# Optimization experiments

Hardware: AMD Instinct MI355X
Metric: run time of the kernel (lower is better)

The kernel has to match this reference:

```python
import jax, jax.numpy as jnp
import numpy as np

B, L, IN_DIM, D, H = 4, 1024, 256, 512, 8
DH = D // H
LARGE_NEG = -10000.0
LN_EPS = 1e-5


def _layernorm(x, g, b):
    mu = jnp.mean(x, axis=-1, keepdims=True)
    var = jnp.mean((x - mu) ** 2, axis=-1, keepdims=True)
    return (x - mu) * jax.lax.rsqrt(var + LN_EPS) * g + b


def setup_inputs() -> dict:
    key = jax.random.key(0)
    ks = jax.random.split(key, 16)
    s = 0.02
    return {
        "x": jax.random.normal(ks[0], (B, L, IN_DIM), jnp.float32),
        "attention_mask": jax.random.bernoulli(ks[1], 0.5, (B, L, L)),
        "adjacency_matrix": jax.random.uniform(ks[2], (B, L, L), jnp.float32),
        "W_fuse": jax.random.normal(ks[3], (D, IN_DIM), jnp.float32) * s,
        "b_fuse": jnp.zeros((D,), jnp.float32),
        "in_proj_w": jax.random.normal(ks[4], (3 * D, D), jnp.float32) * s,
        "in_proj_b": jnp.zeros((3 * D,), jnp.float32),
        "out_w": jax.random.normal(ks[5], (D, D), jnp.float32) * s,
        "out_b": jnp.zeros((D,), jnp.float32),
        "ln1_g": jnp.ones((D,), jnp.float32),
        "ln1_b": jnp.zeros((D,), jnp.float32),
        "ln2_g": jnp.ones((D,), jnp.float32),
        "ln2_b": jnp.zeros((D,), jnp.float32),
        "W1": jax.random.normal(ks[6], (4 * D, D), jnp.float32) * s,
        "b1": jnp.zeros((4 * D,), jnp.float32),
        "W2": jax.random.normal(ks[7], (D, 4 * D), jnp.float32) * s,
        "b2": jnp.zeros((D,), jnp.float32),
        "log_scale": jnp.array(0.0, jnp.float32),  # log(adj_bias_strength=1.0)
    }


def reference(x, attention_mask, adjacency_matrix, W_fuse, b_fuse, in_proj_w,
              in_proj_b, out_w, out_b, ln1_g, ln1_b, ln2_g, ln2_b,
              W1, b1, W2, b2, log_scale):
    # fuse projection (in_dim != d_model)
    x = jnp.einsum("bli,di->bld", x, W_fuse) + b_fuse

    # ensure_self_loops_in_mask: unmask diagonal of fully-masked rows
    eye = jnp.eye(L, dtype=bool)
    row_all = jnp.all(attention_mask, axis=-1)  # [B, L]
    mask = attention_mask & ~(eye[None, :, :] & row_all[:, :, None])

    # additive attention bias: large_neg where masked + scaled clipped adjacency
    bias = jnp.where(mask, LARGE_NEG, 0.0) + \
        jnp.exp(log_scale) * jnp.clip(adjacency_matrix, 0.0, 1.0)  # [B, L, L]

    # --- attention block (pre-norm) ---
    x_norm = _layernorm(x, ln1_g, ln1_b)
    qkv = jnp.einsum("bld,ed->ble", x_norm, in_proj_w) + in_proj_b
    q, k, v = jnp.split(qkv, 3, axis=-1)
    q = q.reshape(B, L, H, DH).transpose(0, 2, 1, 3)  # [B,H,L,DH]
    k = k.reshape(B, L, H, DH).transpose(0, 2, 1, 3)
    v = v.reshape(B, L, H, DH).transpose(0, 2, 1, 3)
    scores = jnp.einsum("bhqd,bhkd->bhqk", q, k) / np.sqrt(DH) + bias[:, None]
    probs = jax.nn.softmax(scores, axis=-1)
    ctx = jnp.einsum("bhqk,bhkd->bhqd", probs, v)
    ctx = ctx.transpose(0, 2, 1, 3).reshape(B, L, D)
    attn_out = jnp.einsum("bld,ed->ble", ctx, out_w) + out_b
    x = x + attn_out

    # --- FFN block (pre-norm) ---
    x_norm = _layernorm(x, ln2_g, ln2_b)
    h = jax.nn.gelu(jnp.einsum("bld,fd->blf", x_norm, W1) + b1, approximate=False)
    ff = jnp.einsum("blf,df->bld", h, W2) + b2
    return x + ff
```

## Files before the change

### kernel.cpp

```cpp
#include <hip/hip_runtime.h>
#include <math.h>

typedef unsigned short UST;
typedef __attribute__((ext_vector_type(8))) short bf16x8;
typedef __attribute__((ext_vector_type(4))) float f32x4;

#define BB 4
#define LL 1024
#define IND 256
#define DD 512
#define HH 8
#define FFD 2048
#define NT (BB*LL)

__device__ __forceinline__ float bf2f(UST u){ return __uint_as_float(((unsigned)u)<<16); }
__device__ __forceinline__ UST f2bf(float f){
  unsigned u = __float_as_uint(f);
  u += 0x7FFFu + ((u>>16)&1u);
  return (UST)(u>>16);
}
__device__ __forceinline__ float ldF(const void* p, long i, int isf32){
  return isf32 ? ((const float*)p)[i] : bf2f(((const UST*)p)[i]);
}
__device__ __forceinline__ bool ldMask(const void* p, long i, int fm){
  if (fm==0) return ((const int*)p)[i] != 0;
  if (fm==1) return ((const unsigned char*)p)[i] != 0;
  if (fm==2) return ((const UST*)p)[i] != 0;
  return ((const float*)p)[i] != 0.f;
}
__device__ __forceinline__ f32x4 mfma16(bf16x8 a, bf16x8 b, f32x4 c){
  return __builtin_amdgcn_mfma_f32_16x16x32_bf16(a, b, c, 0, 0, 0);
}
__device__ __forceinline__ void gld16(const void* g, void* l){
  __builtin_amdgcn_global_load_lds((const __attribute__((address_space(1))) unsigned int*)g,
                                   (__attribute__((address_space(3))) unsigned int*)l, 16, 0, 0);
}

struct CvtArgs { const void* src[11]; UST* dst[11]; int n[11]; };
__global__ __launch_bounds__(256) void prep_k(int* flags, CvtArgs a,
    const UST* xh, const void* mask, const void* adj, const void* lsp, UST* biasOut){
  int bid = blockIdx.x;
  int t = threadIdx.x;
  __shared__ UST sTile[1024];
  __shared__ int sAll[4];
  __shared__ int sFlags[2];
  if (t < 64){
    int lane = t;
    int e0 = (xh[lane] >> 7) & 0xFF;
    int e1 = (xh[64+lane] >> 7) & 0xFF;
    int f32 = __any((e0 >= 140) || (e1 >= 140)) ? 1 : 0;
    unsigned v = ((const unsigned int*)mask)[lane];
    int w01   = __all(v <= 1u) ? 1 : 0;
    unsigned lo = v & 0xFFFFu, hi = v >> 16;
    int half  = __all((lo==0u||lo==0x3F80u) && (hi==0u||hi==0x3F80u)) ? 1 : 0;
    int wordF = __all(v==0u || v==0x3F800000u) ? 1 : 0;
    int byteB = __all((v & 0xFEFEFEFEu) == 0u) ? 1 : 0;
    if (lane == 0){
      int fm = w01 ? 0 : (half ? (wordF ? 3 : 2) : (byteB ? 1 : 0));
      sFlags[0] = f32; sFlags[1] = fm;
      if (bid == 0){ flags[0] = f32; flags[1] = fm; }
    }
  }
  __syncthreads();
  int fF = sFlags[0], fM = sFlags[1];
  if (bid < BB*LL){
    int row = bid;
    int i = row & (LL-1);
    long base = (long)row * LL;
    int j0 = t*4;
    bool mv[4];
    if (fM == 0){
      int4 m4 = *(const int4*)((const int*)mask + base + j0);
      mv[0]=m4.x!=0; mv[1]=m4.y!=0; mv[2]=m4.z!=0; mv[3]=m4.w!=0;
    } else {
      #pragma unroll
      for (int k=0;k<4;++k) mv[k] = ldMask(mask, base + j0 + k, fM);
    }
    float a4[4];
    if (fF){
      float4 av = *(const float4*)((const float*)adj + base + j0);
      a4[0]=av.x; a4[1]=av.y; a4[2]=av.z; a4[3]=av.w;
    } else {
      const UST* ap = (const UST*)adj + base + j0;
      #pragma unroll
      for (int k=0;k<4;++k) a4[k] = bf2f(ap[k]);
    }
    int my = (mv[0]&&mv[1]&&mv[2]&&mv[3]) ? 1 : 0;
    int wa = __all(my);
    int w = t >> 6;
    if ((t & 63) == 0) sAll[w] = wa;
    __syncthreads();
    int rowAll = sAll[0] & sAll[1] & sAll[2] & sAll[3];
    float es = expf(ldF(lsp, 0, fF));
    UST o4[4];
    #pragma unroll
    for (int k = 0; k < 4; ++k){
      int j = j0 + k;
      float av = fminf(fmaxf(a4[k], 0.f), 1.f);
      bool eff = mv[k] && !((rowAll != 0) && (j == i));
      o4[k] = f2bf(((eff ? -10000.f : 0.f) + es * av) * 1.44269504f);
    }
    *(int2*)&sTile[j0] = *(const int2*)o4;
    __syncthreads();
    int kt = t >> 4, l15 = t & 15;
    UST g4[4];
    #pragma unroll
    for (int ni=0; ni<4; ++ni) g4[ni] = sTile[kt*64 + ni*16 + l15];
    int b = row >> 10, rr = row & 1023;
    int qt = rr >> 6, q = rr & 63;
    int w2 = q >> 4, qd = (q >> 2) & 3, r = q & 3;
    long dst = ((long)((b*16 + qt)*16 + kt))*4096 + w2*1024 + (qd*16 + l15)*16 + r*4;
    *(int2*)(biasOut + dst) = *(const int2*)g4;
  } else {
    int cb = bid - BB*LL;
    int ti = cb >> 9, xi = cb & 511;
    int n = a.n[ti];
    long i8 = ((long)xi*256 + t)*8;
    if (i8 >= n) return;
    const void* s = a.src[ti]; UST* d = a.dst[ti];
    if (fF){
      const float4* sf = (const float4*)s;
      float4 a0 = sf[i8>>2], a1 = sf[(i8>>2)+1];
      UST o[8] = { f2bf(a0.x),f2bf(a0.y),f2bf(a0.z),f2bf(a0.w),
                   f2bf(a1.x),f2bf(a1.y),f2bf(a1.z),f2bf(a1.w) };
      *(int4*)(d+i8) = *(const int4*)o;
    } else {
      ((int4*)d)[i8>>3] = ((const int4*)s)[i8>>3];
    }
  }
}

template<int TM, int TN, int ACT, int RES, int OUTMODE>
__global__ __launch_bounds__(256) void gemm3_k(const int* flags,
    const UST* __restrict__ A, const UST* __restrict__ Bw, const UST* __restrict__ bias,
    const float* __restrict__ resid, void* Cout, int M, int N, int K, int Ks){
  constexpr int MI = TM/32, NI = TN/32;
  __shared__ UST sA[2][TM*64];
  __shared__ UST sB[2][TN*64];
  int t = threadIdx.x, w = t>>6, lane = t&63, l15 = lane&15, qd = lane>>4;
  int m0 = blockIdx.x*TM, n0 = blockIdx.y*TN;
  int zoff = blockIdx.z * Ks;
  int wm = (w&1)*(TM/2), wn = (w>>1)*(TN/2);
  f32x4 acc[MI][NI];
  #pragma unroll
  for (int mi=0; mi<MI; ++mi)
    #pragma unroll
    for (int ni=0; ni<NI; ++ni){ acc[mi][ni][0]=0;acc[mi][ni][1]=0;acc[mi][ni][2]=0;acc[mi][ni][3]=0; }
  int sRow = lane&7, sCol = (lane>>3)*8;
  const UST* aS = A + (long)(m0 + w*(TM/4) + sRow)*K + sCol + zoff;
  const UST* bS = Bw + (long)(n0 + w*(TN/4) + sRow)*K + sCol + zoff;
  auto stage = [&](int buf, int k0){
    #pragma unroll
    for (int c=0;c<MI;++c) gld16(aS + (long)c*8*K + k0, (char*)&sA[buf][(w*(TM/4)+c*8)*64]);
    #pragma unroll
    for (int c=0;c<NI;++c) gld16(bS + (long)c*8*K + k0, (char*)&sB[buf][(w*(TN/4)+c*8)*64]);
  };
  stage(0, 0);
  for (int k0 = 0; k0 < Ks; k0 += 64){
    int cur = (k0>>6)&1, nxt = cur^1;
    __syncthreads();
    if (k0 + 64 < Ks) stage(nxt, k0+64);
    #pragma unroll
    for (int ks=0; ks<2; ++ks){
      bf16x8 afr[MI], bfr[NI];
      #pragma unroll
      for (int mi=0; mi<MI; ++mi){
        int R = wm + mi*16 + l15;
        afr[mi] = *(const bf16x8*)&sA[cur][(R>>3)*512 + (ks*4+qd)*64 + (R&7)*8];
      }
      #pragma unroll
      for (int ni=0; ni<NI; ++ni){
        int R = wn + ni*16 + l15;
        bfr[ni] = *(const bf16x8*)&sB[cur][(R>>3)*512 + (ks*4+qd)*64 + (R&7)*8];
      }
      #pragma unroll
      for (int mi=0; mi<MI; ++mi)
        #pragma unroll
        for (int ni=0; ni<NI; ++ni)
          acc[mi][ni] = mfma16(afr[mi], bfr[ni], acc[mi][ni]);
    }
  }
  if (OUTMODE == 3){
    float* P = (float*)Cout + (size_t)blockIdx.z * M * N;
    #pragma unroll
    for (int mi=0; mi<MI; ++mi)
      #pragma unroll
      for (int ni=0; ni<NI; ++ni){
        int gc = n0 + wn + ni*16 + l15;
        #pragma unroll
        for (int r=0; r<4; ++r){
          int grow = m0 + wm + mi*16 + qd*4 + r;
          P[(long)grow*N + gc] = acc[mi][ni][r];
        }
      }
    return;
  }
  int outF32 = (OUTMODE==1) || (OUTMODE==2 && flags[0]);
  #pragma unroll
  for (int mi=0; mi<MI; ++mi){
    #pragma unroll
    for (int ni=0; ni<NI; ++ni){
      int gc = n0 + wn + ni*16 + l15;
      float bv = bf2f(bias[gc]);
      #pragma unroll
      for (int r=0; r<4; ++r){
        int grow = m0 + wm + mi*16 + qd*4 + r;
        float c = acc[mi][ni][r] + bv;
        if (ACT) c = 0.5f*c*(1.f+erff(c*0.70710678118654752f));
        long oi = (long)grow*N + gc;
        if (RES) c += resid[oi];
        if (outF32) ((float*)Cout)[oi] = c;
        else ((UST*)Cout)[oi] = f2bf(c);
      }
    }
  }
}

__global__ __launch_bounds__(256) void reduce4_k(const int* flags,
    const float* __restrict__ parts, const UST* __restrict__ bias,
    const float* __restrict__ resid, void* __restrict__ dout){
  const long S = (long)NT*DD;
  long e = ((long)blockIdx.x*256 + threadIdx.x)*4;
  float4 a = *(const float4*)(parts + e);
  float4 b = *(const float4*)(parts + S + e);
  float4 c = *(const float4*)(parts + 2*S + e);
  float4 d = *(const float4*)(parts + 3*S + e);
  float4 r = *(const float4*)(resid + e);
  int gc = (int)(e & (DD-1));
  float v[4] = { a.x+b.x+c.x+d.x + bf2f(bias[gc+0]) + r.x,
                 a.y+b.y+c.y+d.y + bf2f(bias[gc+1]) + r.y,
                 a.z+b.z+c.z+d.z + bf2f(bias[gc+2]) + r.z,
                 a.w+b.w+c.w+d.w + bf2f(bias[gc+3]) + r.w };
  if (flags[0]){
    *(float4*)((float*)dout + e) = *(const float4*)v;
  } else {
    UST o4[4] = { f2bf(v[0]), f2bf(v[1]), f2bf(v[2]), f2bf(v[3]) };
    *(int2*)((UST*)dout + e) = *(const int2*)o4;
  }
}

__global__ __launch_bounds__(256) void ln_k(const int* flags, const float* xin,
    const void* gp, const void* bp, UST* xout){
  int fF = flags[0];
  int row = blockIdx.x, t = threadIdx.x;
  const float* xr = xin + (long)row * DD;
  float v0 = xr[t], v1 = xr[t+256];
  float s = v0+v1, q = v0*v0 + v1*v1;
  #pragma unroll
  for (int off=1; off<64; off<<=1){ s += __shfl_xor(s,off,64); q += __shfl_xor(q,off,64); }
  __shared__ float rs[4], rq[4];
  int w = t>>6;
  if ((t&63)==0){ rs[w]=s; rq[w]=q; }
  __syncthreads();
  float S = rs[0]+rs[1]+rs[2]+rs[3];
  float Q = rq[0]+rq[1]+rq[2]+rq[3];
  float mean = S * (1.f/DD);
  float var  = fmaxf(Q * (1.f/DD) - mean*mean, 0.f);
  float ri = rsqrtf(var + 1e-5f);
  float g0 = ldF(gp, t, fF), b0 = ldF(bp, t, fF);
  float g1 = ldF(gp, t+256, fF), b1 = ldF(bp, t+256, fF);
  xout[(long)row*DD + t]     = f2bf((v0-mean)*ri*g0 + b0);
  xout[(long)row*DD + t+256] = f2bf((v1-mean)*ri*g1 + b1);
}

__global__ __launch_bounds__(256) void repack_v(const UST* __restrict__ qkv, UST* __restrict__ vT){
  int id = blockIdx.x;
  int bh = id & 31, qt = id >> 5;
  int b = bh >> 3, h = bh & 7;
  int t = threadIdx.x, w = t >> 6, lane = t & 63;
  int token = qt*64 + lane;
  const UST* src = qkv + ((long)(b*LL + token))*1536 + 1024 + h*64;
  #pragma unroll
  for (int c = 0; c < 2; ++c){
    int ch = w*2 + c;
    union { int4 v; UST u[8]; } uu;
    uu.v = *(const int4*)(src + ch*8);
    #pragma unroll
    for (int i = 0; i < 8; ++i)
      vT[((long)(bh*64 + ch*8 + i))*LL + token] = uu.u[i];
  }
}

__global__ __launch_bounds__(256) void attn_k(const UST* __restrict__ qkv,
    const UST* __restrict__ vT, const UST* __restrict__ bias2, UST* __restrict__ ctx){
  int id = blockIdx.x;
  int b = id & 3, h = (id>>2) & 7, qt = id >> 5;
  int bh = b*HH + h;
  int q0 = qt*64;
  int t = threadIdx.x, w = t>>6, lane = t&63, l15 = lane&15, qd = lane>>4;
  __shared__ UST sK[2][2][64*32];
  __shared__ UST sV[2][2][64*32];
  __shared__ UST sP[4][16*72];
  UST* myP = &sP[w][0];

  const UST* qrow = qkv + ((long)(b*LL + q0 + w*16 + l15))*1536 + h*64;
  bf16x8 qf0 = *(const bf16x8*)(qrow + qd*8);
  bf16x8 qf1 = *(const bf16x8*)(qrow + 32 + qd*8);

  const UST* kS = qkv + (long)(b*LL + w*16 + (lane&15))*1536 + 512 + h*64 + (lane>>4)*8;
  const UST* vS = vT + (long)(bh*64 + w*16 + (lane&15))*LL + (lane>>4)*8;
  const UST* bP = bias2 + ((long)((b*16 + qt)*16))*4096 + w*1024 + lane*16;

  f32x4 o[4]; float lsum[4];
  #pragma unroll
  for (int i=0;i<4;i++){ o[i][0]=0;o[i][1]=0;o[i][2]=0;o[i][3]=0; lsum[i]=0.f; }
  const float C1 = 0.18033688f;

  auto stage = [&](int buf, int k0){
    gld16(kS + (long)k0*1536,      (char*)sK[buf][0] + w*1024);
    gld16(kS + (long)k0*1536 + 32, (char*)sK[buf][1] + w*1024);
    gld16(vS + k0,                 (char*)sV[buf][0] + w*1024);
    gld16(vS + k0 + 32,            (char*)sV[buf][1] + w*1024);
  };
  stage(0, 0);
  int4 bc0 = *(const int4*)(bP);
  int4 bc1 = *(const int4*)(bP + 8);

  for (int kt = 0; kt < 16; ++kt){
    int cur = kt&1, nxt = cur^1;
    int k0 = kt*64;
    __syncthreads();
    if (kt < 15) stage(nxt, k0+64);
    int kn = (kt < 15 ? kt+1 : 15);
    int4 bn0 = *(const int4*)(bP + (long)kn*4096);
    int4 bn1 = *(const int4*)(bP + (long)kn*4096 + 8);
    f32x4 s4[4];
    #pragma unroll
    for (int i=0;i<4;i++){ s4[i][0]=0;s4[i][1]=0;s4[i][2]=0;s4[i][3]=0; }
    #pragma unroll
    for (int ni=0; ni<4; ++ni){
      bf16x8 kf0 = *(const bf16x8*)&sK[cur][0][ni*512 + qd*128 + l15*8];
      bf16x8 kf1 = *(const bf16x8*)&sK[cur][1][ni*512 + qd*128 + l15*8];
      s4[ni] = mfma16(qf0, kf0, s4[ni]);
      s4[ni] = mfma16(qf1, kf1, s4[ni]);
    }
    union { int4 v; UST u[8]; } B0, B1;
    B0.v = bc0; B1.v = bc1;
    float p[4][4];
    #pragma unroll
    for (int ni=0; ni<4; ++ni){
      #pragma unroll
      for (int r=0; r<4; ++r){
        UST bu = (r < 2) ? B0.u[r*4 + ni] : B1.u[(r&1)*4 + ni];
        p[ni][r] = exp2f(fmaf(s4[ni][r], C1, bf2f(bu)));
      }
    }
    bc0 = bn0; bc1 = bn1;
    #pragma unroll
    for (int r=0; r<4; ++r)
      lsum[r] += (p[0][r]+p[1][r]) + (p[2][r]+p[3][r]);
    #pragma unroll
    for (int ni=0; ni<4; ++ni)
      #pragma unroll
      for (int r=0; r<4; ++r) myP[(qd*4+r)*72 + ni*16 + l15] = f2bf(p[ni][r]);
    bf16x8 pf0 = *(const bf16x8*)&myP[l15*72 + qd*8];
    bf16x8 pf1 = *(const bf16x8*)&myP[l15*72 + 32 + qd*8];
    #pragma unroll
    for (int dn=0; dn<4; ++dn){
      bf16x8 vf0 = *(const bf16x8*)&sV[cur][0][dn*512 + qd*128 + l15*8];
      bf16x8 vf1 = *(const bf16x8*)&sV[cur][1][dn*512 + qd*128 + l15*8];
      o[dn] = mfma16(pf0, vf0, o[dn]);
      o[dn] = mfma16(pf1, vf1, o[dn]);
    }
  }
  float linv[4];
  #pragma unroll
  for (int r=0; r<4; ++r){
    float s = lsum[r];
    #pragma unroll
    for (int off=1; off<16; off<<=1) s += __shfl_xor(s, off, 64);
    linv[r] = 1.f / s;
  }
  #pragma unroll
  for (int dn=0; dn<4; ++dn){
    #pragma unroll
    for (int r=0; r<4; ++r){
      long oi = ((long)(b*LL + q0 + w*16 + qd*4 + r))*DD + h*64 + dn*16 + l15;
      ctx[oi] = f2bf(o[dn][r] * linv[r]);
    }
  }
}

extern "C" void kernel_launch(void* const* d_in, const int* in_sizes, int n_in,
                              void* d_out, int out_size, void* d_ws, size_t ws_size,
                              hipStream_t stream){
  char* ws = (char*)d_ws;
  size_t o = 0;
  auto alloc = [&](size_t b){ size_t r = o; o += (b + 255) & ~(size_t)255; return r; };
  int*   flags = (int*)(ws + alloc(256));
  size_t biasOff = alloc(8UL<<20);
  size_t qkvOff  = alloc(12UL<<20);
  UST* biasC = (UST*)(ws + biasOff);
  UST* qkv   = (UST*)(ws + qkvOff);
  UST* hb    = (UST*)(ws + biasOff);
  UST* vT    = (UST*)(ws + alloc(4UL<<20));
  UST* xbf   = (UST*)(ws + alloc(2UL<<20));
  UST* wfuse = (UST*)(ws + alloc(131072*2));
  UST* bfuse = (UST*)(ws + alloc(1024));
  UST* ipw   = (UST*)(ws + alloc(786432*2));
  UST* ipb   = (UST*)(ws + alloc(3072*2));
  UST* outw  = (UST*)(ws + alloc(262144*2));
  UST* outb  = (UST*)(ws + alloc(1024));
  UST* w1    = (UST*)(ws + alloc(1048576*2));
  UST* b1    = (UST*)(ws + alloc(4096*2));
  UST* w2    = (UST*)(ws + alloc(1048576*2));
  UST* b2    = (UST*)(ws + alloc(1024));
  float* xf  = (float*)(ws + alloc((size_t)NT*DD*4));
  UST* xn    = (UST*)(ws + alloc((size_t)NT*DD*2));
  UST* ctx   = (UST*)(ws + alloc((size_t)NT*DD*2));
  float* x2  = (float*)(ws + alloc((size_t)NT*DD*4));
  size_t partsOff = alloc(4UL*NT*DD*4);
  float* parts = (float*)(ws + partsOff);
  bool doSplit = (o <= ws_size);

  CvtArgs ca;
  const int srcIdx[11] = {0,3,4,5,6,7,8,13,14,15,16};
  UST* dsts[11] = {xbf,wfuse,bfuse,ipw,ipb,outw,outb,w1,b1,w2,b2};
  const int ns[11] = {NT*IND, DD*IND, DD, 3*DD*DD, 3*DD, DD*DD, DD, FFD*DD, FFD, DD*FFD, DD};
  for (int i=0;i<11;i++){ ca.src[i]=d_in[srcIdx[i]]; ca.dst[i]=dsts[i]; ca.n[i]=ns[i]; }
  prep_k<<<BB*LL + 11*512, 256, 0, stream>>>(flags, ca, (const UST*)d_in[0],
                                             d_in[1], d_in[2], d_in[17], biasC);

  gemm3_k<64,64,0,0,1><<<dim3(64,8), 256, 0, stream>>>(flags, xbf, wfuse, bfuse, nullptr, xf, NT, DD, IND, IND);
  ln_k<<<NT, 256, 0, stream>>>(flags, xf, d_in[9], d_in[10], xn);
  gemm3_k<64,128,0,0,0><<<dim3(64,12), 256, 0, stream>>>(flags, xn, ipw, ipb, nullptr, qkv, NT, 3*DD, DD, DD);
  repack_v<<<512, 256, 0, stream>>>(qkv, vT);
  attn_k<<<512, 256, 0, stream>>>(qkv, vT, biasC, ctx);
  gemm3_k<64,64,0,1,1><<<dim3(64,8), 256, 0, stream>>>(flags, ctx, outw, outb, xf, x2, NT, DD, DD, DD);
  ln_k<<<NT, 256, 0, stream>>>(flags, x2, d_in[11], d_in[12], xn);
  gemm3_k<128,128,1,0,0><<<dim3(32,16), 256, 0, stream>>>(flags, xn, w1, b1, nullptr, hb, NT, FFD, DD, DD);
  if (doSplit){
    gemm3_k<128,128,0,0,3><<<dim3(32,4,4), 256, 0, stream>>>(flags, hb, w2, b2, nullptr, parts, NT, DD, FFD, FFD/4);
    reduce4_k<<<(NT*DD)/1024, 256, 0, stream>>>(flags, parts, b2, x2, d_out);
  } else {
    gemm3_k<64,64,0,1,2><<<dim3(64,8), 256, 0, stream>>>(flags, hb, w2, b2, x2, d_out, NT, DD, FFD, FFD);
  }
}
```

Baseline: 262.3 us.

## Fuse all stages into one cooperative persistent kernel with grid syncs

Replaces the chain of separate kernel launches (prep, GEMMs, layernorms, V repack, attention, split-K reduce) with a single cooperative kernel of 512 blocks. The stages are separated by grid-wide barriers, and each block works through its share of tiles using a shared 64KB LDS buffer. The aim is to remove per-launch overhead and the inter-kernel gaps. In exchange, a fixed 512-block grid with launch_bounds(256,2) caps occupancy, every grid.sync costs a barrier, and stages with more natural tiles (e.g. prep with ~9.7k rows) become strided loops. The old multi-kernel path stays as a fallback if the cooperative launch fails.

```diff
diff --git a/kernel.cpp b/kernel.cpp
--- a/kernel.cpp
+++ b/kernel.cpp
@@ -1,5 +1,8 @@
 #include <hip/hip_runtime.h>
+#include <hip/hip_cooperative_groups.h>
 #include <math.h>
+
+namespace cg = cooperative_groups;
 
 typedef unsigned short UST;
 typedef __attribute__((ext_vector_type(8))) short bf16x8;
@@ -36,52 +39,61 @@
                                    (__attribute__((address_space(3))) unsigned int*)l, 16, 0, 0);
 }
 
-struct CvtArgs { const void* src[11]; UST* dst[11]; int n[11]; };
-__global__ __launch_bounds__(256) void prep_k(int* flags, CvtArgs a,
-    const UST* xh, const void* mask, const void* adj, const void* lsp, UST* biasOut){
-  int bid = blockIdx.x;
+struct MegaArgs {
+  const void* src[11]; UST* dst[11]; int n[11];
+  const UST* xh; const void* mask; const void* adj; const void* lsp;
+  const void* ln1g; const void* ln1b; const void* ln2g; const void* ln2b;
+  UST *bias2, *qkv, *vT, *xn, *ctx, *hb;
+  UST *xbf, *wfuse, *bfuse, *ipw, *ipb, *outw, *outb, *w1, *b1, *w2, *b2;
+  float *xf, *x2, *parts;
+  void* dout;
+  int* flags;
+};
+
+__device__ __forceinline__ void detect_dev(const UST* xh, const unsigned int* mw, int* sF){
   int t = threadIdx.x;
-  __shared__ UST sTile[1024];
-  __shared__ int sAll[4];
-  __shared__ int sFlags[2];
   if (t < 64){
-    int lane = t;
-    int e0 = (xh[lane] >> 7) & 0xFF;
-    int e1 = (xh[64+lane] >> 7) & 0xFF;
+    int e0 = (xh[t] >> 7) & 0xFF;
+    int e1 = (xh[64+t] >> 7) & 0xFF;
     int f32 = __any((e0 >= 140) || (e1 >= 140)) ? 1 : 0;
-    unsigned v = ((const unsigned int*)mask)[lane];
+    unsigned v = mw[t];
     int w01   = __all(v <= 1u) ? 1 : 0;
     unsigned lo = v & 0xFFFFu, hi = v >> 16;
     int half  = __all((lo==0u||lo==0x3F80u) && (hi==0u||hi==0x3F80u)) ? 1 : 0;
     int wordF = __all(v==0u || v==0x3F800000u) ? 1 : 0;
     int byteB = __all((v & 0xFEFEFEFEu) == 0u) ? 1 : 0;
-    if (lane == 0){
-      int fm = w01 ? 0 : (half ? (wordF ? 3 : 2) : (byteB ? 1 : 0));
-      sFlags[0] = f32; sFlags[1] = fm;
-      if (bid == 0){ flags[0] = f32; flags[1] = fm; }
-    }
-  }
-  __syncthreads();
-  int fF = sFlags[0], fM = sFlags[1];
-  if (bid < BB*LL){
-    int row = bid;
+    if (t == 0){
+      sF[0] = f32;
+      sF[1] = w01 ? 0 : (half ? (wordF ? 3 : 2) : (byteB ? 1 : 0));
+    }
+  }
+}
+
+__device__ __forceinline__ void prep_item(char* smemc, int fF, int fM,
+    const MegaArgs& a, int idx){
+  int t = threadIdx.x;
+  UST* sTile = (UST*)smemc;
+  int* sAll  = (int*)(smemc + 2048);
+  __syncthreads();
+  if (idx < BB*LL){
+    int row = idx;
     int i = row & (LL-1);
     long base = (long)row * LL;
     int j0 = t*4;
     bool mv[4];
     if (fM == 0){
-      int4 m4 = *(const int4*)((const int*)mask + base + j0);
+      int4 m4 = *(const int4*)((const int*)a.mask + base + j0);
       mv[0]=m4.x!=0; mv[1]=m4.y!=0; mv[2]=m4.z!=0; mv[3]=m4.w!=0;
     } else {
       #pragma unroll
-      for (int k=0;k<4;++k) mv[k] = ldMask(mask, base + j0 + k, fM);
+      for (int k=0;k<4;++k) mv[k] = ldMask(a.mask, base + j0 + k, fM);
     }
     float a4[4];
     if (fF){
-      float4 av = *(const float4*)((const float*)adj + base + j0);
+      float4 av = *(const float4*)((const float*)a.adj + base + j0);
       a4[0]=av.x; a4[1]=av.y; a4[2]=av.z; a4[3]=av.w;
     } else {
-      const UST* ap = (const UST*)adj + base + j0;
+      const UST* ap = (const UST*)a.adj + base + j0;
       #pragma unroll
       for (int k=0;k<4;++k) a4[k] = bf2f(ap[k]);
     }
@@ -91,7 +103,7 @@
     if ((t & 63) == 0) sAll[w] = wa;
     __syncthreads();
     int rowAll = sAll[0] & sAll[1] & sAll[2] & sAll[3];
-    float es = expf(ldF(lsp, 0, fF));
+    float es = expf(ldF(a.lsp, 0, fF));
     UST o4[4];
     #pragma unroll
     for (int k = 0; k < 4; ++k){
@@ -110,36 +122,37 @@
     int qt = rr >> 6, q = rr & 63;
     int w2 = q >> 4, qd = (q >> 2) & 3, r = q & 3;
     long dst = ((long)((b*16 + qt)*16 + kt))*4096 + w2*1024 + (qd*16 + l15)*16 + r*4;
-    *(int2*)(biasOut + dst) = *(const int2*)g4;
+    *(int2*)(a.bias2 + dst) = *(const int2*)g4;
   } else {
-    int cb = bid - BB*LL;
+    int cb = idx - BB*LL;
     int ti = cb >> 9, xi = cb & 511;
     int n = a.n[ti];
     long i8 = ((long)xi*256 + t)*8;
-    if (i8 >= n) return;
-    const void* s = a.src[ti]; UST* d = a.dst[ti];
-    if (fF){
-      const float4* sf = (const float4*)s;
-      float4 a0 = sf[i8>>2], a1 = sf[(i8>>2)+1];
-      UST o[8] = { f2bf(a0.x),f2bf(a0.y),f2bf(a0.z),f2bf(a0.w),
-                   f2bf(a1.x),f2bf(a1.y),f2bf(a1.z),f2bf(a1.w) };
-      *(int4*)(d+i8) = *(const int4*)o;
-    } else {
-      ((int4*)d)[i8>>3] = ((const int4*)s)[i8>>3];
+    if (i8 < n){
+      const void* s = a.src[ti]; UST* d = a.dst[ti];
+      if (fF){
+        const float4* sf = (const float4*)s;
+        float4 a0 = sf[i8>>2], a1 = sf[(i8>>2)+1];
+        UST o[8] = { f2bf(a0.x),f2bf(a0.y),f2bf(a0.z),f2bf(a0.w),
+                     f2bf(a1.x),f2bf(a1.y),f2bf(a1.z),f2bf(a1.w) };
+        *(int4*)(d+i8) = *(const int4*)o;
+      } else {
+        ((int4*)d)[i8>>3] = ((const int4*)s)[i8>>3];
+      }
     }
   }
 }
 
 template<int TM, int TN, int ACT, int RES, int OUTMODE>
-__global__ __launch_bounds__(256) void gemm3_k(const int* flags,
+__device__ __forceinline__ void gemm_tile(char* smemc, int fF,
     const UST* __restrict__ A, const UST* __restrict__ Bw, const UST* __restrict__ bias,
-    const float* __restrict__ resid, void* Cout, int M, int N, int K, int Ks){
+    const float* __restrict__ resid, void* Cout,
+    int M, int N, int K, int Ks, int m0, int n0, int zslice){
   constexpr int MI = TM/32, NI = TN/32;
-  __shared__ UST sA[2][TM*64];
-  __shared__ UST sB[2][TN*64];
+  UST* sA0 = (UST*)smemc;
+  UST* sB0 = (UST*)(smemc + 2*TM*64*2);
   int t = threadIdx.x, w = t>>6, lane = t&63, l15 = lane&15, qd = lane>>4;
-  int m0 = blockIdx.x*TM, n0 = blockIdx.y*TN;
-  int zoff = blockIdx.z * Ks;
+  int zoff = zslice * Ks;
   int wm = (w&1)*(TM/2), wn = (w>>1)*(TN/2);
   f32x4 acc[MI][NI];
   #pragma unroll
@@ -151,10 +164,11 @@
   const UST* bS = Bw + (long)(n0 + w*(TN/4) + sRow)*K + sCol + zoff;
   auto stage = [&](int buf, int k0){
     #pragma unroll
-    for (int c=0;c<MI;++c) gld16(aS + (long)c*8*K + k0, (char*)&sA[buf][(w*(TM/4)+c*8)*64]);
-    #pragma unroll
-    for (int c=0;c<NI;++c) gld16(bS + (long)c*8*K + k0, (char*)&sB[buf][(w*(TN/4)+c*8)*64]);
+    for (int c=0;c<MI;++c) gld16(aS + (long)c*8*K + k0, (char*)(sA0 + buf*(TM*64) + (w*(TM/4)+c*8)*64));
+    #pragma unroll
+    for (int c=0;c<NI;++c) gld16(bS + (long)c*8*K + k0, (char*)(sB0 + buf*(TN*64) + (w*(TN/4)+c*8)*64));
   };
+  __syncthreads();
   stage(0, 0);
   for (int k0 = 0; k0 < Ks; k0 += 64){
     int cur = (k0>>6)&1, nxt = cur^1;
@@ -166,12 +180,12 @@
       #pragma unroll
       for (int mi=0; mi<MI; ++mi){
         int R = wm + mi*16 + l15;
-        afr[mi] = *(const bf16x8*)&sA[cur][(R>>3)*512 + (ks*4+qd)*64 + (R&7)*8];
+        afr[mi] = *(const bf16x8*)&sA0[cur*(TM*64) + (R>>3)*512 + (ks*4+qd)*64 + (R&7)*8];
       }
       #pragma unroll
       for (int ni=0; ni<NI; ++ni){
         int R = wn + ni*16 + l15;
-        bfr[ni] = *(const bf16x8*)&sB[cur][(R>>3)*512 + (ks*4+qd)*64 + (R&7)*8];
+        bfr[ni] = *(const bf16x8*)&sB0[cur*(TN*64) + (R>>3)*512 + (ks*4+qd)*64 + (R&7)*8];
       }
       #pragma unroll
       for (int mi=0; mi<MI; ++mi)
@@ -181,7 +195,7 @@
     }
   }
   if (OUTMODE == 3){
-    float* P = (float*)Cout + (size_t)blockIdx.z * M * N;
+    float* P = (float*)Cout + (size_t)zslice * M * N;
     #pragma unroll
     for (int mi=0; mi<MI; ++mi)
       #pragma unroll
@@ -195,7 +209,7 @@
       }
     return;
   }
-  int outF32 = (OUTMODE==1) || (OUTMODE==2 && flags[0]);
+  int outF32 = (OUTMODE==1) || (OUTMODE==2 && fF);
   #pragma unroll
   for (int mi=0; mi<MI; ++mi){
     #pragma unroll
@@ -216,11 +230,154 @@
   }
 }
 
-__global__ __launch_bounds__(256) void reduce4_k(const int* flags,
-    const float* __restrict__ parts, const UST* __restrict__ bias,
-    const float* __restrict__ resid, void* __restrict__ dout){
+__device__ __forceinline__ void ln_row(char* smemc, int fF, const float* xin,
+    const void* gp, const void* bp, UST* xout, int row){
+  float* rs = (float*)smemc;
+  float* rq = rs + 4;
+  int t = threadIdx.x;
+  const float* xr = xin + (long)row * DD;
+  float v0 = xr[t], v1 = xr[t+256];
+  float s = v0+v1, q = v0*v0 + v1*v1;
+  #pragma unroll
+  for (int off=1; off<64; off<<=1){ s += __shfl_xor(s,off,64); q += __shfl_xor(q,off,64); }
+  int w = t>>6;
+  __syncthreads();
+  if ((t&63)==0){ rs[w]=s; rq[w]=q; }
+  __syncthreads();
+  float S = rs[0]+rs[1]+rs[2]+rs[3];
+  float Q = rq[0]+rq[1]+rq[2]+rq[3];
+  float mean = S * (1.f/DD);
+  float var  = fmaxf(Q * (1.f/DD) - mean*mean, 0.f);
+  float ri = rsqrtf(var + 1e-5f);
+  float g0 = ldF(gp, t, fF), b0 = ldF(bp, t, fF);
+  float g1 = ldF(gp, t+256, fF), b1 = ldF(bp, t+256, fF);
+  xout[(long)row*DD + t]     = f2bf((v0-mean)*ri*g0 + b0);
+  xout[(long)row*DD + t+256] = f2bf((v1-mean)*ri*g1 + b1);
+}
+
+__device__ __forceinline__ void repack_item(const UST* __restrict__ qkv,
+    UST* __restrict__ vT, int id){
+  int bh = id & 31, qt = id >> 5;
+  int b = bh >> 3, h = bh & 7;
+  int t = threadIdx.x, w = t >> 6, lane = t & 63;
+  int token = qt*64 + lane;
+  const UST* src = qkv + ((long)(b*LL + token))*1536 + 1024 + h*64;
+  #pragma unroll
+  for (int c = 0; c < 2; ++c){
+    int ch = w*2 + c;
+    union { int4 v; UST u[8]; } uu;
+    uu.v = *(const int4*)(src + ch*8);
+    #pragma unroll
+    for (int i = 0; i < 8; ++i)
+      vT[((long)(bh*64 + ch*8 + i))*LL + token] = uu.u[i];
+  }
+}
+
+__device__ __forceinline__ void attn_tile(char* smemc, const UST* __restrict__ qkv,
+    const UST* __restrict__ vT, const UST* __restrict__ bias2, UST* __restrict__ ctx, int id){
+  UST* sK = (UST*)smemc;
+  UST* sV = (UST*)(smemc + 16384);
+  UST* sP = (UST*)(smemc + 32768);
+  int b = id & 3, h = (id>>2) & 7, qt = id >> 5;
+  int bh = b*HH + h;
+  int q0 = qt*64;
+  int t = threadIdx.x, w = t>>6, lane = t&63, l15 = lane&15, qd = lane>>4;
+  UST* myP = sP + w*16*72;
+
+  const UST* qrow = qkv + ((long)(b*LL + q0 + w*16 + l15))*1536 + h*64;
+  bf16x8 qf0 = *(const bf16x8*)(qrow + qd*8);
+  bf16x8 qf1 = *(const bf16x8*)(qrow + 32 + qd*8);
+
+  const UST* kS = qkv + (long)(b*LL + w*16 + l15)*1536 + 512 + h*64 + qd*8;
+  const UST* vS = vT + (long)(bh*64 + w*16 + l15)*LL + qd*8;
+  const UST* bP = bias2 + ((long)((b*16 + qt)*16))*4096 + w*1024 + lane*16;
+
+  f32x4 o[4]; float lsum[4];
+  #pragma unroll
+  for (int i=0;i<4;i++){ o[i][0]=0;o[i][1]=0;o[i][2]=0;o[i][3]=0; lsum[i]=0.f; }
+  const float C1 = 0.18033688f;
+
+  auto stage = [&](int buf, int k0){
+    gld16(kS + (long)k0*1536,      (char*)sK + (buf*2+0)*4096 + w*1024);
+    gld16(kS + (long)k0*1536 + 32, (char*)sK + (buf*2+1)*4096 + w*1024);
+    gld16(vS + k0,                 (char*)sV + (buf*2+0)*4096 + w*1024);
+    gld16(vS + k0 + 32,            (char*)sV + (buf*2+1)*4096 + w*1024);
+  };
+  __syncthreads();
+  stage(0, 0);
+  int4 bc0 = *(const int4*)(bP);
+  int4 bc1 = *(const int4*)(bP + 8);
+
+  for (int kt = 0; kt < 16; ++kt){
+    int cur = kt&1, nxt = cur^1;
+    int k0 = kt*64;
+    __syncthreads();
+    if (kt < 15) stage(nxt, k0+64);
+    int kn = (kt < 15 ? kt+1 : 15);
+    int4 bn0 = *(const int4*)(bP + (long)kn*4096);
+    int4 bn1 = *(const int4*)(bP + (long)kn*4096 + 8);
+    f32x4 s4[4];
+    #pragma unroll
+    for (int i=0;i<4;i++){ s4[i][0]=0;s4[i][1]=0;s4[i][2]=0;s4[i][3]=0; }
+    #pragma unroll
+    for (int ni=0; ni<4; ++ni){
+      bf16x8 kf0 = *(const bf16x8*)&sK[(cur*2+0)*2048 + ni*512 + qd*128 + l15*8];
+      bf16x8 kf1 = *(const bf16x8*)&sK[(cur*2+1)*2048 + ni*512 + qd*128 + l15*8];
+      s4[ni] = mfma16(qf0, kf0, s4[ni]);
+      s4[ni] = mfma16(qf1, kf1, s4[ni]);
+    }
+    union { int4 v; UST u[8]; } B0, B1;
+    B0.v = bc0; B1.v = bc1;
+    float p[4][4];
+    #pragma unroll
+    for (int ni=0; ni<4; ++ni){
+      #pragma unroll
+      for (int r=0; r<4; ++r){
+        UST bu = (r < 2) ? B0.u[r*4 + ni] : B1.u[(r&1)*4 + ni];
+        p[ni][r] = exp2f(fmaf(s4[ni][r], C1, bf2f(bu)));
+      }
+    }
+    bc0 = bn0; bc1 = bn1;
+    #pragma unroll
+    for (int r=0; r<4; ++r)
+      lsum[r] += (p[0][r]+p[1][r]) + (p[2][r]+p[3][r]);
+    #pragma unroll
+    for (int ni=0; ni<4; ++ni)
+      #pragma unroll
+      for (int r=0; r<4; ++r) myP[(qd*4+r)*72 + ni*16 + l15] = f2bf(p[ni][r]);
+    bf16x8 pf0 = *(const bf16x8*)&myP[l15*72 + qd*8];
+    bf16x8 pf1 = *(const bf16x8*)&myP[l15*72 + 32 + qd*8];
+    #pragma unroll
+    for (int dn=0; dn<4; ++dn){
+      bf16x8 vf0 = *(const bf16x8*)&sV[(cur*2+0)*2048 + dn*512 + qd*128 + l15*8];
+      bf16x8 vf1 = *(const bf16x8*)&sV[(cur*2+1)*2048 + dn*512 + qd*128 + l15*8];
+      o[dn] = mfma16(pf0, vf0, o[dn]);
+      o[dn] = mfma16(pf1, vf1, o[dn]);
+    }
+  }
+  float linv[4];
+  #pragma unroll
+  for (int r=0; r<4; ++r){
+    float s = lsum[r];
+    #pragma unroll
+    for (int off=1; off<16; off<<=1) s += __shfl_xor(s, off, 64);
+    linv[r] = 1.f / s;
+  }
+  #pragma unroll
+  for (int dn=0; dn<4; ++dn){
+    #pragma unroll
+    for (int r=0; r<4; ++r){
+      long oi = ((long)(b*LL + q0 + w*16 + qd*4 + r))*DD + h*64 + dn*16 + l15;
+      ctx[oi] = f2bf(o[dn][r] * linv[r]);
+    }
+  }
+}
+
+__device__ __forceinline__ void reduce_item(int fF, const float* __restrict__ parts,
+    const UST* __restrict__ bias, const float* __restrict__ resid,
+    void* __restrict__ dout, int blk){
   const long S = (long)NT*DD;
-  long e = ((long)blockIdx.x*256 + threadIdx.x)*4;
+  long e = ((long)blk*256 + threadIdx.x)*4;
   float4 a = *(const float4*)(parts + e);
   float4 b = *(const float4*)(parts + S + e);
   float4 c = *(const float4*)(parts + 2*S + e);
@@ -231,7 +388,7 @@
                  a.y+b.y+c.y+d.y + bf2f(bias[gc+1]) + r.y,
                  a.z+b.z+c.z+d.z + bf2f(bias[gc+2]) + r.z,
                  a.w+b.w+c.w+d.w + bf2f(bias[gc+3]) + r.w };
-  if (flags[0]){
+  if (fF){
     *(float4*)((float*)dout + e) = *(const float4*)v;
   } else {
     UST o4[4] = { f2bf(v[0]), f2bf(v[1]), f2bf(v[2]), f2bf(v[3]) };
@@ -239,146 +396,86 @@
   }
 }
 
+__global__ __launch_bounds__(256, 2) void mega_k(MegaArgs a){
+  __shared__ char smem[65536];
+  cg::grid_group grid = cg::this_grid();
+  int bid = blockIdx.x;
+  int* sF = (int*)(smem + 8192);
+  detect_dev(a.xh, (const unsigned int*)a.mask, sF);
+  __syncthreads();
+  int fF = sF[0], fM = sF[1];
+  if (bid == 0 && threadIdx.x == 0){ a.flags[0] = fF; a.flags[1] = fM; }
+
+  for (int idx = bid; idx < BB*LL + 11*512; idx += 512)
+    prep_item(smem, fF, fM, a, idx);
+  grid.sync();
+  gemm_tile<64,64,0,0,1>(smem, fF, a.xbf, a.wfuse, a.bfuse, nullptr, a.xf,
+                         NT, DD, IND, IND, (bid>>3)*64, (bid&7)*64, 0);
+  grid.sync();
+  for (int i=0;i<8;++i) ln_row(smem, fF, a.xf, a.ln1g, a.ln1b, a.xn, bid + i*512);
+  grid.sync();
+  for (int idx = bid; idx < 768; idx += 512)
+    gemm_tile<64,128,0,0,0>(smem, fF, a.xn, a.ipw, a.ipb, nullptr, a.qkv,
+                            NT, 3*DD, DD, DD, (idx & 63)*64, (idx >> 6)*128, 0);
+  grid.sync();
+  repack_item(a.qkv, a.vT, bid);
+  grid.sync();
+  attn_tile(smem, a.qkv, a.vT, a.bias2, a.ctx, bid);
+  grid.sync();
+  gemm_tile<64,64,0,1,1>(smem, fF, a.ctx, a.outw, a.outb, a.xf, a.x2,
+                         NT, DD, DD, DD, (bid>>3)*64, (bid&7)*64, 0);
+  grid.sync();
+  for (int i=0;i<8;++i) ln_row(smem, fF, a.x2, a.ln2g, a.ln2b, a.xn, bid + i*512);
+  grid.sync();
+  gemm_tile<128,128,1,0,0>(smem, fF, a.xn, a.w1, a.b1, nullptr, a.hb,
+                           NT, FFD, DD, DD, (bid>>4)*128, (bid&15)*128, 0);
+  grid.sync();
+  { int z = bid >> 7, mn = bid & 127;
+    gemm_tile<128,128,0,0,3>(smem, fF, a.hb, a.w2, a.b2, nullptr, a.parts,
+                             NT, DD, FFD, FFD/4, (mn>>2)*128, (mn&3)*128, z); }
+  grid.sync();
+  for (int i=0;i<4;++i) reduce_item(fF, a.parts, a.b2, a.x2, a.dout, bid + i*512);
+}
+
+__global__ __launch_bounds__(256) void prep_k(MegaArgs a){
+  __shared__ char smem[4096];
+  int* sF = (int*)(smem + 2560);
+  detect_dev(a.xh, (const unsigned int*)a.mask, sF);
+  __syncthreads();
+  int fF = sF[0], fM = sF[1];
+  if (blockIdx.x == 0 && threadIdx.x == 0){ a.flags[0] = fF; a.flags[1] = fM; }
+  prep_item(smem, fF, fM, a, blockIdx.x);
+}
+
+template<int TM, int TN, int ACT, int RES, int OUTMODE>
+__global__ __launch_bounds__(256) void gemm3_k(const int* flags,
+    const UST* A, const UST* Bw, const UST* bias, const float* resid, void* Cout,
+    int M, int N, int K, int Ks){
+  __shared__ char smem[2*TM*64*2 + 2*TN*64*2];
+  int fF = (OUTMODE==2) ? flags[0] : 0;
+  gemm_tile<TM,TN,ACT,RES,OUTMODE>(smem, fF, A, Bw, bias, resid, Cout,
+      M, N, K, Ks, blockIdx.x*TM, blockIdx.y*TN, blockIdx.z);
+}
+
 __global__ __launch_bounds__(256) void ln_k(const int* flags, const float* xin,
     const void* gp, const void* bp, UST* xout){
-  int fF = flags[0];
-  int row = blockIdx.x, t = threadIdx.x;
-  const float* xr = xin + (long)row * DD;
-  float v0 = xr[t], v1 = xr[t+256];
-  float s = v0+v1, q = v0*v0 + v1*v1;
-  #pragma unroll
-  for (int off=1; off<64; off<<=1){ s += __shfl_xor(s,off,64); q += __shfl_xor(q,off,64); }
-  __shared__ float rs[4], rq[4];
-  int w = t>>6;
-  if ((t&63)==0){ rs[w]=s; rq[w]=q; }
-  __syncthreads();
-  float S = rs[0]+rs[1]+rs[2]+rs[3];
-  float Q = rq[0]+rq[1]+rq[2]+rq[3];
-  float mean = S * (1.f/DD);
-  float var  = fmaxf(Q * (1.f/DD) - mean*mean, 0.f);
-  float ri = rsqrtf(var + 1e-5f);
-  float g0 = ldF(gp, t, fF), b0 = ldF(bp, t, fF);
-  float g1 = ldF(gp, t+256, fF), b1 = ldF(bp, t+256, fF);
-  xout[(long)row*DD + t]     = f2bf((v0-mean)*ri*g0 + b0);
-  xout[(long)row*DD + t+256] = f2bf((v1-mean)*ri*g1 + b1);
-}
-
-__global__ __launch_bounds__(256) void repack_v(const UST* __restrict__ qkv, UST* __restrict__ vT){
-  int id = blockIdx.x;
-  int bh = id & 31, qt = id >> 5;
-  int b = bh >> 3, h = bh & 7;
-  int t = threadIdx.x, w = t >> 6, lane = t & 63;
-  int token = qt*64 + lane;
-  const UST* src = qkv + ((long)(b*LL + token))*1536 + 1024 + h*64;
-  #pragma unroll
-  for (int c = 0; c < 2; ++c){
-    int ch = w*2 + c;
-    union { int4 v; UST u[8]; } uu;
-    uu.v = *(const int4*)(src + ch*8);
-    #pragma unroll
-    for (int i = 0; i < 8; ++i)
-      vT[((long)(bh*64 + ch*8 + i))*LL + token] = uu.u[i];
-  }
-}
-
-__global__ __launch_bounds__(256) void attn_k(const UST* __restrict__ qkv,
-    const UST* __restrict__ vT, const UST* __restrict__ bias2, UST* __restrict__ ctx){
-  int id = blockIdx.x;
-  int b = id & 3, h = (id>>2) & 7, qt = id >> 5;
-  int bh = b*HH + h;
-  int q0 = qt*64;
-  int t = threadIdx.x, w = t>>6, lane = t&63, l15 = lane&15, qd = lane>>4;
-  __shared__ UST sK[2][2][64*32];
-  __shared__ UST sV[2][2][64*32];
-  __shared__ UST sP[4][16*72];
-  UST* myP = &sP[w][0];
-
-  const UST* qrow = qkv + ((long)(b*LL + q0 + w*16 + l15))*1536 + h*64;
-  bf16x8 qf0 = *(const bf16x8*)(qrow + qd*8);
-  bf16x8 qf1 = *(const bf16x8*)(qrow + 32 + qd*8);
-
-  const UST* kS = qkv + (long)(b*LL + w*16 + (lane&15))*1536 + 512 + h*64 + (lane>>4)*8;
-  const UST* vS = vT + (long)(bh*64 + w*16 + (lane&15))*LL + (lane>>4)*8;
-  const UST* bP = bias2 + ((long)((b*16 + qt)*16))*4096 + w*1024 + lane*16;
-
-  f32x4 o[4]; float lsum[4];
-  #pragma unroll
-  for (int i=0;i<4;i++){ o[i][0]=0;o[i][1]=0;o[i][2]=0;o[i][3]=0; lsum[i]=0.f; }
-  const float C1 = 0.18033688f;
-
-  auto stage = [&](int buf, int k0){
-    gld16(kS + (long)k0*1536,      (char*)sK[buf][0] + w*1024);
-    gld16(kS + (long)k0*1536 + 32, (char*)sK[buf][1] + w*1024);
-    gld16(vS + k0,                 (char*)sV[buf][0] + w*1024);
-    gld16(vS + k0 + 32,            (char*)sV[buf][1] + w*1024);
-  };
-  stage(0, 0);
-  int4 bc0 = *(const int4*)(bP);
-  int4 bc1 = *(const int4*)(bP + 8);
-
-  for (int kt = 0; kt < 16; ++kt){
-    int cur = kt&1, nxt = cur^1;
-    int k0 = kt*64;
-    __syncthreads();
-    if (kt < 15) stage(nxt, k0+64);
-    int kn = (kt < 15 ? kt+1 : 15);
-    int4 bn0 = *(const int4*)(bP + (long)kn*4096);
-    int4 bn1 = *(const int4*)(bP + (long)kn*4096 + 8);
-    f32x4 s4[4];
-    #pragma unroll
-    for (int i=0;i<4;i++){ s4[i][0]=0;s4[i][1]=0;s4[i][2]=0;s4[i][3]=0; }
-    #pragma unroll
-    for (int ni=0; ni<4; ++ni){
-      bf16x8 kf0 = *(const bf16x8*)&sK[cur][0][ni*512 + qd*128 + l15*8];
-      bf16x8 kf1 = *(const bf16x8*)&sK[cur][1][ni*512 + qd*128 + l15*8];
-      s4[ni] = mfma16(qf0, kf0, s4[ni]);
-      s4[ni] = mfma16(qf1, kf1, s4[ni]);
-    }
-    union { int4 v; UST u[8]; } B0, B1;
-    B0.v = bc0; B1.v = bc1;
-    float p[4][4];
-    #pragma unroll
-    for (int ni=0; ni<4; ++ni){
-      #pragma unroll
-      for (int r=0; r<4; ++r){
-        UST bu = (r < 2) ? B0.u[r*4 + ni] : B1.u[(r&1)*4 + ni];
-        p[ni][r] = exp2f(fmaf(s4[ni][r], C1, bf2f(bu)));
-      }
-    }
-    bc0 = bn0; bc1 = bn1;
-    #pragma unroll
-    for (int r=0; r<4; ++r)
-      lsum[r] += (p[0][r]+p[1][r]) + (p[2][r]+p[3][r]);
-    #pragma unroll
-    for (int ni=0; ni<4; ++ni)
-      #pragma unroll
-      for (int r=0; r<4; ++r) myP[(qd*4+r)*72 + ni*16 + l15] = f2bf(p[ni][r]);
-    bf16x8 pf0 = *(const bf16x8*)&myP[l15*72 + qd*8];
-    bf16x8 pf1 = *(const bf16x8*)&myP[l15*72 + 32 + qd*8];
-    #pragma unroll
-    for (int dn=0; dn<4; ++dn){
-      bf16x8 vf0 = *(const bf16x8*)&sV[cur][0][dn*512 + qd*128 + l15*8];
-      bf16x8 vf1 = *(const bf16x8*)&sV[cur][1][dn*512 + qd*128 + l15*8];
-      o[dn] = mfma16(pf0, vf0, o[dn]);
-      o[dn] = mfma16(pf1, vf1, o[dn]);
-    }
-  }
-  float linv[4];
-  #pragma unroll
-  for (int r=0; r<4; ++r){
-    float s = lsum[r];
-    #pragma unroll
-    for (int off=1; off<16; off<<=1) s += __shfl_xor(s, off, 64);
-    linv[r] = 1.f / s;
-  }
-  #pragma unroll
-  for (int dn=0; dn<4; ++dn){
-    #pragma unroll
-    for (int r=0; r<4; ++r){
-      long oi = ((long)(b*LL + q0 + w*16 + qd*4 + r))*DD + h*64 + dn*16 + l15;
-      ctx[oi] = f2bf(o[dn][r] * linv[r]);
-    }
-  }
+  __shared__ char smem[64];
+  ln_row(smem, flags[0], xin, gp, bp, xout, blockIdx.x);
+}
+
+__global__ __launch_bounds__(256) void repack_v(const UST* qkv, UST* vT){
+  repack_item(qkv, vT, blockIdx.x);
+}
+
+__global__ __launch_bounds__(256) void attn_k(const UST* qkv, const UST* vT,
+    const UST* bias2, UST* ctx){
+  __shared__ char smem[41472];
+  attn_tile(smem, qkv, vT, bias2, ctx, blockIdx.x);
+}
+
+__global__ __launch_bounds__(256) void reduce4_k(const int* flags, const float* parts,
+    const UST* bias, const float* resid, void* dout){
+  reduce_item(flags[0], parts, bias, resid, dout, blockIdx.x);
 }
 
 extern "C" void kernel_launch(void* const* d_in, const int* in_sizes, int n_in,
@@ -411,28 +508,43 @@
   float* x2  = (float*)(ws + alloc((size_t)NT*DD*4));
   size_t partsOff = alloc(4UL*NT*DD*4);
   float* parts = (float*)(ws + partsOff);
-  bool doSplit = (o <= ws_size);
-
-  CvtArgs ca;
+  bool fits = (o <= ws_size);
+
+  MegaArgs ma;
   const int srcIdx[11] = {0,3,4,5,6,7,8,13,14,15,16};
   UST* dsts[11] = {xbf,wfuse,bfuse,ipw,ipb,outw,outb,w1,b1,w2,b2};
   const int ns[11] = {NT*IND, DD*IND, DD, 3*DD*DD, 3*DD, DD*DD, DD, FFD*DD, FFD, DD*FFD, DD};
-  for (int i=0;i<11;i++){ ca.src[i]=d_in[srcIdx[i]]; ca.dst[i]=dsts[i]; ca.n[i]=ns[i]; }
-  prep_k<<<BB*LL + 11*512, 256, 0, stream>>>(flags, ca, (const UST*)d_in[0],
-                                             d_in[1], d_in[2], d_in[17], biasC);
-
-  gemm3_k<64,64,0,0,1><<<dim3(64,8), 256, 0, stream>>>(flags, xbf, wfuse, bfuse, nullptr, xf, NT, DD, IND, IND);
-  ln_k<<<NT, 256, 0, stream>>>(flags, xf, d_in[9], d_in[10], xn);
-  gemm3_k<64,128,0,0,0><<<dim3(64,12), 256, 0, stream>>>(flags, xn, ipw, ipb, nullptr, qkv, NT, 3*DD, DD, DD);
-  repack_v<<<512, 256, 0, stream>>>(qkv, vT);
-  attn_k<<<512, 256, 0, stream>>>(qkv, vT, biasC, ctx);
-  gemm3_k<64,64,0,1,1><<<dim3(64,8), 256, 0, stream>>>(flags, ctx, outw, outb, xf, x2, NT, DD, DD, DD);
-  ln_k<<<NT, 256, 0, stream>>>(flags, x2, d_in[11], d_in[12], xn);
-  gemm3_k<128,128,1,0,0><<<dim3(32,16), 256, 0, stream>>>(flags, xn, w1, b1, nullptr, hb, NT, FFD, DD, DD);
-  if (doSplit){
-    gemm3_k<128,128,0,0,3><<<dim3(32,4,4), 256, 0, stream>>>(flags, hb, w2, b2, nullptr, parts, NT, DD, FFD, FFD/4);
-    reduce4_k<<<(NT*DD)/1024, 256, 0, stream>>>(flags, parts, b2, x2, d_out);
-  } else {
-    gemm3_k<64,64,0,1,2><<<dim3(64,8), 256, 0, stream>>>(flags, hb, w2, b2, x2, d_out, NT, DD, FFD, FFD);
-  }
-}
+  for (int i=0;i<11;i++){ ma.src[i]=d_in[srcIdx[i]]; ma.dst[i]=dsts[i]; ma.n[i]=ns[i]; }
+  ma.xh = (const UST*)d_in[0];
+  ma.mask = d_in[1]; ma.adj = d_in[2]; ma.lsp = d_in[17];
+  ma.ln1g = d_in[9]; ma.ln1b = d_in[10]; ma.ln2g = d_in[11]; ma.ln2b = d_in[12];
+  ma.bias2 = biasC; ma.qkv = qkv; ma.vT = vT; ma.xn = xn; ma.ctx = ctx; ma.hb = hb;
+  ma.xbf=xbf; ma.wfuse=wfuse; ma.bfuse=bfuse; ma.ipw=ipw; ma.ipb=ipb;
+  ma.outw=outw; ma.outb=outb; ma.w1=w1; ma.b1=b1; ma.w2=w2; ma.b2=b2;
+  ma.xf = xf; ma.x2 = x2; ma.parts = parts;
+  ma.dout = d_out; ma.flags = flags;
+
+  hipError_t err = hipErrorUnknown;
+  if (fits){
+    void* params[] = { (void*)&ma };
+    err = hipLaunchCooperativeKernel((const void*)mega_k, dim3(512), dim3(256),
+                                     params, 0, stream);
+  }
+  if (err != hipSuccess){
+    prep_k<<<BB*LL + 11*512, 256, 0, stream>>>(ma);
+    gemm3_k<64,64,0,0,1><<<dim3(64,8), 256, 0, stream>>>(flags, xbf, wfuse, bfuse, nullptr, xf, NT, DD, IND, IND);
+    ln_k<<<NT, 256, 0, stream>>>(flags, xf, d_in[9], d_in[10], xn);
+    gemm3_k<64,128,0,0,0><<<dim3(64,12), 256, 0, stream>>>(flags, xn, ipw, ipb, nullptr, qkv, NT, 3*DD, DD, DD);
+    repack_v<<<512, 256, 0, stream>>>(qkv, vT);
+    attn_k<<<512, 256, 0, stream>>>(qkv, vT, biasC, ctx);
+    gemm3_k<64,64,0,1,1><<<dim3(64,8), 256, 0, stream>>>(flags, ctx, outw, outb, xf, x2, NT, DD, DD, DD);
+    ln_k<<<NT, 256, 0, stream>>>(flags, x2, d_in[11], d_in[12], xn);
+    gemm3_k<128,128,1,0,0><<<dim3(32,16), 256, 0, stream>>>(flags, xn, w1, b1, nullptr, hb, NT, FFD, DD, DD);
+    if (fits){
+      gemm3_k<128,128,0,0,3><<<dim3(32,4,4), 256, 0, stream>>>(flags, hb, w2, b2, nullptr, parts, NT, DD, FFD, FFD/4);
+      reduce4_k<<<(NT*DD)/1024, 256, 0, stream>>>(flags, parts, b2, x2, d_out);
+    } else {
+      gemm3_k<64,64,0,1,2><<<dim3(64,8), 256, 0, stream>>>(flags, hb, w2, b2, x2, d_out, NT, DD, FFD, FFD);
+    }
+  }
+}
```

Result: slower. 885.9 us (+237.8%).
